# Kernel tuning notes

Measured on AMD Instinct MI355X. Metric: run time of the kernel, lower is better.

The kernel has to match this reference:

```python
import jax, jax.numpy as jnp
import numpy as np

N = 100000
E = 1600000
F_IN = 128
HID = 64
HEADS = 2
OUT_HEADS = 1
NUM_CLASS = 18
NEG_SLOPE = 0.2


def setup_inputs() -> dict:
    key = jax.random.key(0)
    ks = jax.random.split(key, 12)
    x = jax.random.normal(ks[0], (N, F_IN), dtype=jnp.float32)
    edge_index = jax.random.randint(ks[1], (2, E), 0, N, dtype=jnp.int64)
    s = lambda k, shp, fan: jax.random.normal(k, shp, dtype=jnp.float32) * (1.0 / np.sqrt(fan))
    W0 = s(ks[2], (F_IN, HID), F_IN)
    b0 = jnp.zeros((HID,), dtype=jnp.float32)
    W1 = s(ks[3], (HID, HEADS * HID), HID)
    att_src1 = s(ks[4], (HEADS, HID), HID)
    att_dst1 = s(ks[5], (HEADS, HID), HID)
    b1 = jnp.zeros((HEADS * HID,), dtype=jnp.float32)
    W2 = s(ks[6], (HEADS * HID, OUT_HEADS * NUM_CLASS), HEADS * HID)
    att_src2 = s(ks[7], (OUT_HEADS, NUM_CLASS), NUM_CLASS)
    att_dst2 = s(ks[8], (OUT_HEADS, NUM_CLASS), NUM_CLASS)
    b2 = jnp.zeros((OUT_HEADS * NUM_CLASS,), dtype=jnp.float32)
    return {"x": x, "edge_index": edge_index, "W0": W0, "b0": b0,
            "W1": W1, "att_src1": att_src1, "att_dst1": att_dst1, "b1": b1,
            "W2": W2, "att_src2": att_src2, "att_dst2": att_dst2, "b2": b2}


def gat_conv(x, src, dst, W, att_s, att_d, bias, heads, out_ch):
    n = x.shape[0]
    h = (x @ W).reshape(n, heads, out_ch)              # [N,H,C]
    a_s = jnp.sum(h * att_s, axis=-1)                   # [N,H]
    a_d = jnp.sum(h * att_d, axis=-1)                   # [N,H]
    e = jax.nn.leaky_relu(a_s[src] + a_d[dst], NEG_SLOPE)  # [E,H]
    m = jax.ops.segment_max(e, dst, num_segments=n)
    ex = jnp.exp(e - m[dst])
    denom = jax.ops.segment_sum(ex, dst, num_segments=n)
    alpha = ex / denom[dst]                              # [E,H]
    msg = h[src] * alpha[:, :, None]                     # [E,H,C]
    out = jax.ops.segment_sum(msg, dst, num_segments=n)  # [N,H,C]
    return out.reshape(n, heads * out_ch) + bias


def reference(x, edge_index, W0, b0, W1, att_src1, att_dst1, b1, W2, att_src2, att_dst2, b2):
    n = x.shape[0]
    # PyG GATConv adds self-loops by default
    loops = jnp.arange(n, dtype=edge_index.dtype)
    src = jnp.concatenate([edge_index[0], loops])
    dst = jnp.concatenate([edge_index[1], loops])
    # eval mode: dropout is identity
    h = jax.nn.relu(x @ W0 + b0)
    h = jax.nn.elu(gat_conv(h, src, dst, W1, att_src1, att_dst1, b1, HEADS, HID))
    out = gat_conv(h, src, dst, W2, att_src2, att_dst2, b2, OUT_HEADS, NUM_CLASS)
    return jax.nn.log_softmax(out, axis=-1)
```

## Files before the change

kernel.cpp:

```cpp
#include <hip/hip_runtime.h>
#include <math.h>


#define NEG_SLOPE 0.2f
#define STASH_CAP 128

typedef unsigned short ushort_t;

__device__ __forceinline__ float wmax(float v) {
    for (int o = 32; o; o >>= 1) v = fmaxf(v, __shfl_xor(v, o));
    return v;
}
__device__ __forceinline__ float wsum(float v) {
    for (int o = 32; o; o >>= 1) v += __shfl_xor(v, o);
    return v;
}

__device__ __forceinline__ unsigned bfpack(float a, float b) {
    unsigned ua = __float_as_uint(a);
    unsigned ub = __float_as_uint(b);
    ua = (ua + 0x7fffu + ((ua >> 16) & 1u)) >> 16;
    ub = (ub + 0x7fffu + ((ub >> 16) & 1u)) & 0xffff0000u;
    return ua | ub;
}
__device__ __forceinline__ ushort_t bf16of(float a) {
    unsigned ua = __float_as_uint(a);
    return (ushort_t)((ua + 0x7fffu + ((ua >> 16) & 1u)) >> 16);
}
__device__ __forceinline__ float bflo(unsigned u) { return __uint_as_float(u << 16); }
__device__ __forceinline__ float bfhi(unsigned u) { return __uint_as_float(u & 0xffff0000u); }
__device__ __forceinline__ float bfval(ushort_t u) { return __uint_as_float(((unsigned)u) << 16); }

__global__ void k_deg_init(int* __restrict__ deg, int N) {
    int i = blockIdx.x * blockDim.x + threadIdx.x;
    if (i < N) deg[i] = 1;
}
__global__ void k_deg_edges(const int* __restrict__ ei, int* __restrict__ deg,
                            int* __restrict__ eofs, int E) {
    int e = blockIdx.x * blockDim.x + threadIdx.x;
    if (e < E) eofs[e] = atomicAdd(&deg[ei[E + e]], 1);
}

__global__ __launch_bounds__(256) void k_scan1(const int* __restrict__ deg, int* __restrict__ rs,
                                               int* __restrict__ bsum, int N) {
    __shared__ int s[256];
    int t = threadIdx.x;
    int base = blockIdx.x * 1024;
    int i0 = base + t * 4;
    int d0 = (i0 + 0 < N) ? deg[i0 + 0] : 0;
    int d1 = (i0 + 1 < N) ? deg[i0 + 1] : 0;
    int d2 = (i0 + 2 < N) ? deg[i0 + 2] : 0;
    int d3 = (i0 + 3 < N) ? deg[i0 + 3] : 0;
    int s0 = d0, s1 = s0 + d1, s2 = s1 + d2, s3 = s2 + d3;
    int tsum = s3;
    s[t] = tsum;
    __syncthreads();
    for (int off = 1; off < 256; off <<= 1) {
        int v = (t >= off) ? s[t - off] : 0;
        __syncthreads();
        s[t] += v;
        __syncthreads();
    }
    int excl = s[t] - tsum;
    if (i0 + 0 < N) rs[1 + i0 + 0] = excl + s0;
    if (i0 + 1 < N) rs[1 + i0 + 1] = excl + s1;
    if (i0 + 2 < N) rs[1 + i0 + 2] = excl + s2;
    if (i0 + 3 < N) rs[1 + i0 + 3] = excl + s3;
    if (t == 0) bsum[blockIdx.x] = s[255];
}

__global__ __launch_bounds__(256) void k_scan2(const int* __restrict__ bsum,
                                               int* __restrict__ boff, int NB) {
    __shared__ int s[256];
    int t = threadIdx.x;
    int orig = (t < NB) ? bsum[t] : 0;
    s[t] = orig;
    __syncthreads();
    for (int off = 1; off < 256; off <<= 1) {
        int v = (t >= off) ? s[t - off] : 0;
        __syncthreads();
        s[t] += v;
        __syncthreads();
    }
    if (t < NB) boff[t] = s[t] - orig;
}

__global__ void k_scan3(int* __restrict__ rs, const int* __restrict__ boff, int N) {
    int i = blockIdx.x * blockDim.x + threadIdx.x;
    if (i == 0) rs[0] = 0;
    if (i < N) rs[1 + i] += boff[i >> 10];
}

__global__ __launch_bounds__(256) void k_scatter(const int* __restrict__ ei,
                                                 const int* __restrict__ eofs,
                                                 const int* __restrict__ rs,
                                                 int* __restrict__ csr,
                                                 int E, int Etot, int cohortBlocks) {
    int c = blockIdx.x & 7;
    int pb = blockIdx.x >> 3;
    int tid = pb * 256 + threadIdx.x;
    int stride = cohortBlocks * 256;
    for (int e = tid; e < Etot; e += stride) {
        int dst = (e < E) ? ei[E + e] : (e - E);
        if (((dst >> 13) & 7) != c) continue;
        int src, ofs;
        if (e < E) { src = ei[e]; ofs = eofs[e]; } else { src = dst; ofs = 0; }
        csr[rs[dst] + ofs] = src;
    }
}


__global__ __launch_bounds__(256) void k_gemm1(const float* __restrict__ x,
                                               const float* __restrict__ W0,
                                               const float* __restrict__ b0,
                                               unsigned* __restrict__ h0b, int N) {
    __shared__ float wl[128 * 64];
    __shared__ float al[64 * 132];
    int t = threadIdx.x;
    int n0 = blockIdx.x * 64;
    const float4* wg = (const float4*)W0;
    float4* wl4 = (float4*)wl;
#pragma unroll
    for (int i = 0; i < 8; ++i) wl4[t + i * 256] = wg[t + i * 256];
#pragma unroll
    for (int i = 0; i < 8; ++i) {
        int f = t + i * 256;
        int node = f >> 5, q = f & 31;
        int ng = n0 + node; if (ng > N - 1) ng = N - 1;
        float4 v = ((const float4*)x)[(size_t)ng * 32 + q];
        *(float4*)&al[node * 132 + q * 4] = v;
    }
    __syncthreads();
    int colg = t & 15;
    int rowg = t >> 4;
    float4 acc[4];
#pragma unroll
    for (int j = 0; j < 4; ++j) acc[j] = make_float4(0.f, 0.f, 0.f, 0.f);
    for (int k4 = 0; k4 < 128; k4 += 4) {
        float4 w0 = *(float4*)&wl[(k4 + 0) * 64 + colg * 4];
        float4 w1 = *(float4*)&wl[(k4 + 1) * 64 + colg * 4];
        float4 w2 = *(float4*)&wl[(k4 + 2) * 64 + colg * 4];
        float4 w3 = *(float4*)&wl[(k4 + 3) * 64 + colg * 4];
#pragma unroll
        for (int j = 0; j < 4; ++j) {
            float4 a = *(float4*)&al[(rowg * 4 + j) * 132 + k4];
            acc[j].x += a.x * w0.x + a.y * w1.x + a.z * w2.x + a.w * w3.x;
            acc[j].y += a.x * w0.y + a.y * w1.y + a.z * w2.y + a.w * w3.y;
            acc[j].z += a.x * w0.z + a.y * w1.z + a.z * w2.z + a.w * w3.z;
            acc[j].w += a.x * w0.w + a.y * w1.w + a.z * w2.w + a.w * w3.w;
        }
    }
    float4 bb = ((const float4*)b0)[colg];
#pragma unroll
    for (int j = 0; j < 4; ++j) {
        int n = n0 + rowg * 4 + j;
        if (n < N) {
            float rx = fmaxf(acc[j].x + bb.x, 0.f);
            float ry = fmaxf(acc[j].y + bb.y, 0.f);
            float rz = fmaxf(acc[j].z + bb.z, 0.f);
            float rw = fmaxf(acc[j].w + bb.w, 0.f);
            uint2 pr; pr.x = bfpack(rx, ry); pr.y = bfpack(rz, rw);
            ((uint2*)h0b)[(size_t)n * 16 + colg] = pr;
        }
    }
}

__global__ __launch_bounds__(256) void k_gemm2(const unsigned* __restrict__ h0b,
                                               const float* __restrict__ W1,
                                               const float* __restrict__ as_g,
                                               const float* __restrict__ ad_g,
                                               ushort_t* __restrict__ h1b,
                                               float* __restrict__ as1,
                                               float* __restrict__ ad1, int N) {
    __shared__ float wl[64 * 128];
    __shared__ float al[64 * 68];
    int t = threadIdx.x;
    int n0 = blockIdx.x * 64;
    const float4* wg = (const float4*)W1;
    float4* wl4 = (float4*)wl;
#pragma unroll
    for (int i = 0; i < 8; ++i) wl4[t + i * 256] = wg[t + i * 256];
#pragma unroll
    for (int i = 0; i < 2; ++i) {
        int f = t + i * 256;
        int node = f >> 3, q = f & 7;
        int ng = n0 + node; if (ng > N - 1) ng = N - 1;
        uint4 u = ((const uint4*)h0b)[(size_t)ng * 8 + q];
        float* dst = &al[node * 68 + q * 8];
        dst[0] = bflo(u.x); dst[1] = bfhi(u.x);
        dst[2] = bflo(u.y); dst[3] = bfhi(u.y);
        dst[4] = bflo(u.z); dst[5] = bfhi(u.z);
        dst[6] = bflo(u.w); dst[7] = bfhi(u.w);
    }
    __syncthreads();
    int colg = t & 31;
    int rowg = t >> 5;
    float4 acc[8];
#pragma unroll
    for (int j = 0; j < 8; ++j) acc[j] = make_float4(0.f, 0.f, 0.f, 0.f);
    for (int k4 = 0; k4 < 64; k4 += 4) {
        float4 w0 = *(float4*)&wl[(k4 + 0) * 128 + colg * 4];
        float4 w1 = *(float4*)&wl[(k4 + 1) * 128 + colg * 4];
        float4 w2 = *(float4*)&wl[(k4 + 2) * 128 + colg * 4];
        float4 w3 = *(float4*)&wl[(k4 + 3) * 128 + colg * 4];
#pragma unroll
        for (int j = 0; j < 8; ++j) {
            float4 a = *(float4*)&al[(rowg * 8 + j) * 68 + k4];
            acc[j].x += a.x * w0.x + a.y * w1.x + a.z * w2.x + a.w * w3.x;
            acc[j].y += a.x * w0.y + a.y * w1.y + a.z * w2.y + a.w * w3.y;
            acc[j].z += a.x * w0.z + a.y * w1.z + a.z * w2.z + a.w * w3.z;
            acc[j].w += a.x * w0.w + a.y * w1.w + a.z * w2.w + a.w * w3.w;
        }
    }
    float4 asv = ((const float4*)as_g)[colg];
    float4 adv = ((const float4*)ad_g)[colg];
    float ps[8], pd[8];
#pragma unroll
    for (int j = 0; j < 8; ++j) {
        ps[j] = acc[j].x * asv.x + acc[j].y * asv.y + acc[j].z * asv.z + acc[j].w * asv.w;
        pd[j] = acc[j].x * adv.x + acc[j].y * adv.y + acc[j].z * adv.z + acc[j].w * adv.w;
    }
    for (int o = 1; o < 16; o <<= 1) {
#pragma unroll
        for (int j = 0; j < 8; ++j) {
            ps[j] += __shfl_xor(ps[j], o);
            pd[j] += __shfl_xor(pd[j], o);
        }
    }
#pragma unroll
    for (int j = 0; j < 8; ++j) {
        int n = n0 + rowg * 8 + j;
        if (n < N) {
            uint2 pr;
            pr.x = bfpack(acc[j].x, acc[j].y);
            pr.y = bfpack(acc[j].z, acc[j].w);
            ((uint2*)h1b)[(size_t)n * 32 + colg] = pr;
        }
    }
    int lane = t & 63;
    if ((lane & 15) == 0) {
        int head = (lane >> 4) & 1;
#pragma unroll
        for (int j = 0; j < 8; ++j) {
            int n = n0 + rowg * 8 + j;
            if (n < N) {
                as1[n * 2 + head] = ps[j];
                ad1[n * 2 + head] = pd[j];
            }
        }
    }
}

__global__ __launch_bounds__(256) void k_node_l1(const int* __restrict__ rs,
                                                 const int* __restrict__ csr,
                                                 const ushort_t* __restrict__ h1b,
                                                 const float* __restrict__ as1,
                                                 const float* __restrict__ ad1,
                                                 const float* __restrict__ b1,
                                                 unsigned* __restrict__ aggb, int N) {
    __shared__ float2 stashA[4][128];
    __shared__ float4 stashE[4][STASH_CAP];
    int wid = threadIdx.x >> 6;
    int lane = threadIdx.x & 63;
    int n = (blockIdx.x * 256 + threadIdx.x) >> 6;
    if (n >= N) return;
    int row = rs[n], end = rs[n + 1];
    int deg = end - row;
    float2 adv = ((const float2*)ad1)[n];
    const float2* asp = (const float2*)as1;
    const char* h1base = (const char*)h1b;
    int eg = lane >> 4;
    int fl = lane & 15;
    int head_off = (fl >= 8) ? 64 : 0;
    int flbase = fl * 16;
    float acc[8] = {0.f, 0.f, 0.f, 0.f, 0.f, 0.f, 0.f, 0.f};
    float inv0, inv1;
    if (deg <= 64) {
        bool act = lane < deg;
        int src = act ? csr[row + lane] : 0;
        float2 av = asp[src];
        float e0 = av.x + adv.x, e1 = av.y + adv.y;
        e0 = e0 > 0.f ? e0 : NEG_SLOPE * e0;
        e1 = e1 > 0.f ? e1 : NEG_SLOPE * e1;
        if (!act) { e0 = -INFINITY; e1 = -INFINITY; }
        float m0 = wmax(e0), m1 = wmax(e1);
        float p0 = act ? __expf(e0 - m0) : 0.f;
        float p1 = act ? __expf(e1 - m1) : 0.f;
        inv0 = __builtin_amdgcn_rcpf(wsum(p0));
        inv1 = __builtin_amdgcn_rcpf(wsum(p1));
        stashA[wid][lane] = make_float2(__int_as_float(src), p0);
        stashA[wid][64 + lane] = make_float2(__int_as_float(src), p1);
        int deg8 = (deg + 7) & ~7;
        int b0i = head_off + eg;
        float2 sa0 = stashA[wid][b0i];
        float2 sa1 = stashA[wid][b0i + 4];
        uint4 u0 = *(const uint4*)(h1base + (((unsigned)__float_as_int(sa0.x)) << 8) + flbase);
        uint4 u1 = *(const uint4*)(h1base + (((unsigned)__float_as_int(sa1.x)) << 8) + flbase);
        for (int j = 0; j < deg8; j += 8) {
            int jn = (j + 8 < deg8) ? j + 8 : 0;
            float2 sb0 = stashA[wid][b0i + jn];
            float2 sb1 = stashA[wid][b0i + jn + 4];
            uint4 v0 = *(const uint4*)(h1base + (((unsigned)__float_as_int(sb0.x)) << 8) + flbase);
            uint4 v1 = *(const uint4*)(h1base + (((unsigned)__float_as_int(sb1.x)) << 8) + flbase);
            float a0 = sa0.y, a1 = sa1.y;
            acc[0] += bflo(u0.x) * a0; acc[1] += bfhi(u0.x) * a0;
            acc[2] += bflo(u0.y) * a0; acc[3] += bfhi(u0.y) * a0;
            acc[4] += bflo(u0.z) * a0; acc[5] += bfhi(u0.z) * a0;
            acc[6] += bflo(u0.w) * a0; acc[7] += bfhi(u0.w) * a0;
            acc[0] += bflo(u1.x) * a1; acc[1] += bfhi(u1.x) * a1;
            acc[2] += bflo(u1.y) * a1; acc[3] += bfhi(u1.y) * a1;
            acc[4] += bflo(u1.z) * a1; acc[5] += bfhi(u1.z) * a1;
            acc[6] += bflo(u1.w) * a1; acc[7] += bfhi(u1.w) * a1;
            sa0 = sb0; sa1 = sb1; u0 = v0; u1 = v1;
        }
    } else {
        inv0 = 1.f; inv1 = 1.f;
        float m0 = -INFINITY, m1 = -INFINITY, l0 = 0.f, l1 = 0.f;
        for (int base = row; base < end; base += 64) {
            int idx = base + lane;
            bool act = idx < end;
            int src = act ? csr[idx] : 0;
            float2 av = asp[src];
            float e0 = av.x + adv.x, e1 = av.y + adv.y;
            e0 = e0 > 0.f ? e0 : NEG_SLOPE * e0;
            e1 = e1 > 0.f ? e1 : NEG_SLOPE * e1;
            int sidx = idx - row;
            if (act && sidx < STASH_CAP)
                stashE[wid][sidx] = make_float4(__int_as_float(src), e0, e1, 0.f);
            if (!act) { e0 = -INFINITY; e1 = -INFINITY; }
            float m0n = fmaxf(m0, wmax(e0));
            float m1n = fmaxf(m1, wmax(e1));
            float p0 = act ? __expf(e0 - m0n) : 0.f;
            float p1 = act ? __expf(e1 - m1n) : 0.f;
            l0 = l0 * __expf(m0 - m0n) + wsum(p0);
            l1 = l1 * __expf(m1 - m1n) + wsum(p1);
            m0 = m0n; m1 = m1n;
        }
        float r0 = __builtin_amdgcn_rcpf(l0);
        float r1 = __builtin_amdgcn_rcpf(l1);
        for (int base = row; base < end; base += 64) {
            int idx = base + lane;
            bool act = idx < end;
            int sidx = idx - row;
            int src; float e0, e1;
            if (sidx < STASH_CAP) {
                float4 se = stashE[wid][sidx];
                src = __float_as_int(se.x);
                e0 = se.y; e1 = se.z;
            } else {
                src = act ? csr[idx] : 0;
                float2 av = asp[src];
                e0 = av.x + adv.x; e1 = av.y + adv.y;
                e0 = e0 > 0.f ? e0 : NEG_SLOPE * e0;
                e1 = e1 > 0.f ? e1 : NEG_SLOPE * e1;
            }
            if (!act) src = 0;
            float a0 = act ? __expf(e0 - m0) * r0 : 0.f;
            float a1 = act ? __expf(e1 - m1) * r1 : 0.f;
            stashA[wid][lane] = make_float2(__int_as_float(src), a0);
            stashA[wid][64 + lane] = make_float2(__int_as_float(src), a1);
            int cnt = min(64, end - base);
            for (int j = 0; j < cnt; j += 4) {
                float2 sa = stashA[wid][head_off + j + eg];
                int sj = __float_as_int(sa.x);
                float aj = sa.y;
                uint4 u = *(const uint4*)(h1base + (((unsigned)sj) << 8) + flbase);
                acc[0] += bflo(u.x) * aj; acc[1] += bfhi(u.x) * aj;
                acc[2] += bflo(u.y) * aj; acc[3] += bfhi(u.y) * aj;
                acc[4] += bflo(u.z) * aj; acc[5] += bfhi(u.z) * aj;
                acc[6] += bflo(u.w) * aj; acc[7] += bfhi(u.w) * aj;
            }
        }
    }
#pragma unroll
    for (int i = 0; i < 8; ++i) {
        acc[i] += __shfl_xor(acc[i], 16);
        acc[i] += __shfl_xor(acc[i], 32);
    }
    if (lane < 16) {
        float inv = (lane >= 8) ? inv1 : inv0;
        float4 ba = ((const float4*)b1)[lane * 2];
        float4 bb4 = ((const float4*)b1)[lane * 2 + 1];
        float v[8];
        v[0] = acc[0] * inv + ba.x;  v[1] = acc[1] * inv + ba.y;
        v[2] = acc[2] * inv + ba.z;  v[3] = acc[3] * inv + ba.w;
        v[4] = acc[4] * inv + bb4.x; v[5] = acc[5] * inv + bb4.y;
        v[6] = acc[6] * inv + bb4.z; v[7] = acc[7] * inv + bb4.w;
#pragma unroll
        for (int i = 0; i < 8; ++i) v[i] = v[i] > 0.f ? v[i] : __expf(v[i]) - 1.f;
        uint4 pk;
        pk.x = bfpack(v[0], v[1]); pk.y = bfpack(v[2], v[3]);
        pk.z = bfpack(v[4], v[5]); pk.w = bfpack(v[6], v[7]);
        ((uint4*)aggb)[(size_t)n * 16 + lane] = pk;
    }
}

__global__ __launch_bounds__(256, 4) void k_node2(const unsigned* __restrict__ aggb,
                                                  const float* __restrict__ W2,
                                                  const float* __restrict__ as_g,
                                                  const float* __restrict__ ad_g,
                                                  ushort_t* __restrict__ h2b,
                                                  float* __restrict__ a_s,
                                                  float* __restrict__ a_d, int N) {
    __shared__ float al[64 * 132];
    __shared__ float w2t[20 * 132];
    int t = threadIdx.x;
    int n0 = blockIdx.x * 64;
#pragma unroll
    for (int i = 0; i < 4; ++i) {
        int f = t + i * 256;
        int node = f >> 4, q = f & 15;
        int ng = n0 + node; if (ng > N - 1) ng = N - 1;
        uint4 u = ((const uint4*)aggb)[(size_t)ng * 16 + q];
        float* dst = &al[node * 132 + q * 8];
        dst[0] = bflo(u.x); dst[1] = bfhi(u.x);
        dst[2] = bflo(u.y); dst[3] = bfhi(u.y);
        dst[4] = bflo(u.z); dst[5] = bfhi(u.z);
        dst[6] = bflo(u.w); dst[7] = bfhi(u.w);
    }
    for (int i = t; i < 2560; i += 256) {
        int c = i >> 7, k = i & 127;
        w2t[c * 132 + k] = (c < 18) ? W2[k * 18 + c] : 0.f;
    }
    __syncthreads();
    int node = t >> 2;
    int cq = t & 3;
    int c0 = cq * 5;
    int n = n0 + node;
    float acc[5] = {0.f, 0.f, 0.f, 0.f, 0.f};
#pragma unroll 2
    for (int k4 = 0; k4 < 128; k4 += 4) {
        float4 a = *(float4*)&al[node * 132 + k4];
#pragma unroll
        for (int i = 0; i < 5; ++i) {
            float4 w = *(float4*)&w2t[(c0 + i) * 132 + k4];
            acc[i] += a.x * w.x + a.y * w.y + a.z * w.z + a.w * w.w;
        }
    }
    float ps = 0.f, pd = 0.f;
#pragma unroll
    for (int i = 0; i < 5; ++i) {
        int c = c0 + i;
        float asv = (c < 18) ? as_g[c] : 0.f;
        float adv = (c < 18) ? ad_g[c] : 0.f;
        ps += acc[i] * asv;
        pd += acc[i] * adv;
    }
    ps += __shfl_xor(ps, 1); ps += __shfl_xor(ps, 2);
    pd += __shfl_xor(pd, 1); pd += __shfl_xor(pd, 2);
    if (n < N) {
#pragma unroll
        for (int i = 0; i < 5; ++i) {
            int c = c0 + i;
            if (c < 18) h2b[(size_t)n * 32 + c] = bf16of(acc[i]);
        }
        if (cq == 0) { a_s[n] = ps; a_d[n] = pd; }
    }
}

__global__ __launch_bounds__(256) void k_node_l2(const int* __restrict__ rs,
                                                 const int* __restrict__ csr,
                                                 const ushort_t* __restrict__ h2b,
                                                 const float* __restrict__ as2,
                                                 const float* __restrict__ ad2,
                                                 const float* __restrict__ b2,
                                                 float* __restrict__ out, int N) {
    __shared__ float2 stash[4][STASH_CAP];
    int wid = threadIdx.x >> 6;
    int lane = threadIdx.x & 63;
    int n = (blockIdx.x * 256 + threadIdx.x) >> 6;
    if (n >= N) return;
    int row = rs[n], end = rs[n + 1];
    int deg = end - row;
    float adn = ad2[n];
    int g = lane / 21;
    int c = lane - g * 21;
    int cc = c < 18 ? c : 17;
    float acc = 0.f;
    float post;
    if (deg <= 64) {
        bool act = lane < deg;
        int src = act ? csr[row + lane] : 0;
        float e = as2[src] + adn;
        e = e > 0.f ? e : NEG_SLOPE * e;
        if (!act) e = -INFINITY;
        float m = wmax(e);
        float p = act ? __expf(e - m) : 0.f;
        post = __builtin_amdgcn_rcpf(wsum(p));
        stash[wid][lane] = make_float2(__int_as_float(src), p);
        int o = g;
        for (; o + 3 < deg; o += 6) {
            float2 s0 = stash[wid][o];
            float2 s1 = stash[wid][o + 3];
            int q0 = __float_as_int(s0.x);
            int q1 = __float_as_int(s1.x);
            float v0 = bfval(h2b[(size_t)q0 * 32 + cc]);
            float v1 = bfval(h2b[(size_t)q1 * 32 + cc]);
            acc += s0.y * v0 + s1.y * v1;
        }
        if (o < deg) {
            float2 s0 = stash[wid][o];
            int q0 = __float_as_int(s0.x);
            acc += s0.y * bfval(h2b[(size_t)q0 * 32 + cc]);
        }
    } else {
        post = 1.f;
        float m = -INFINITY, l = 0.f;
        for (int base = row; base < end; base += 64) {
            int idx = base + lane;
            bool act = idx < end;
            int src = act ? csr[idx] : 0;
            float e = as2[src] + adn;
            e = e > 0.f ? e : NEG_SLOPE * e;
            int sidx = idx - row;
            if (act && sidx < STASH_CAP)
                stash[wid][sidx] = make_float2(__int_as_float(src), e);
            if (!act) e = -INFINITY;
            float mn = fmaxf(m, wmax(e));
            float p = act ? __expf(e - mn) : 0.f;
            l = l * __expf(m - mn) + wsum(p);
            m = mn;
        }
        float invl = __builtin_amdgcn_rcpf(l);
        int lim = deg < STASH_CAP ? deg : STASH_CAP;
        for (int o = g; o < lim; o += 3) {
            float2 se = stash[wid][o];
            int src = __float_as_int(se.x);
            float alpha = __expf(se.y - m) * invl;
            acc += alpha * bfval(h2b[(size_t)src * 32 + cc]);
        }
        for (int pos = row + STASH_CAP + g; pos < end; pos += 3) {
            int src = csr[pos];
            float e = as2[src] + adn;
            e = e > 0.f ? e : NEG_SLOPE * e;
            float alpha = __expf(e - m) * invl;
            acc += alpha * bfval(h2b[(size_t)src * 32 + cc]);
        }
    }
    float t1 = __shfl(acc, (lane + 21) & 63);
    float t2 = __shfl(acc, (lane + 42) & 63);
    acc += t1 + t2;
    float bb = (lane < 18) ? b2[lane] : 0.f;
    float v = acc * post + bb;
    float tmx = (lane < 18) ? v : -INFINITY;
    for (int o = 16; o; o >>= 1) tmx = fmaxf(tmx, __shfl_xor(tmx, o));
    float s = (lane < 18) ? __expf(v - tmx) : 0.f;
    for (int o = 16; o; o >>= 1) s += __shfl_xor(s, o);
    float lse = tmx + __logf(s);
    if (lane < 18) out[(size_t)n * 18 + lane] = v - lse;
}

extern "C" void kernel_launch(void* const* d_in, const int* in_sizes, int n_in,
                              void* d_out, int out_size, void* d_ws, size_t ws_size,
                              hipStream_t stream) {
    const float* x      = (const float*)d_in[0];
    const int*   ei     = (const int*)d_in[1];
    const float* W0     = (const float*)d_in[2];
    const float* b0     = (const float*)d_in[3];
    const float* W1     = (const float*)d_in[4];
    const float* att_s1 = (const float*)d_in[5];
    const float* att_d1 = (const float*)d_in[6];
    const float* b1     = (const float*)d_in[7];
    const float* W2     = (const float*)d_in[8];
    const float* att_s2 = (const float*)d_in[9];
    const float* att_d2 = (const float*)d_in[10];
    const float* b2     = (const float*)d_in[11];

    const int N = in_sizes[0] / 128;
    const int E = in_sizes[1] / 2;
    const int Etot = E + N;
    const int NB = (N + 1023) / 1024;
    const int NBLK = (N + 63) / 64;

    char* w = (char*)d_ws;
    unsigned* h0b  = (unsigned*)w; w += (size_t)N * 64 * 2;
    ushort_t* h1b  = (ushort_t*)w; w += (size_t)N * 128 * 2;
    unsigned* aggb = (unsigned*)w; w += (size_t)N * 128 * 2;
    float* as1     = (float*)w;    w += (size_t)N * 2 * 4;
    float* ad1     = (float*)w;    w += (size_t)N * 2 * 4;
    ushort_t* h2b  = (ushort_t*)w; w += (size_t)N * 32 * 2;
    float* as2     = (float*)w;    w += (size_t)N * 4;
    float* ad2     = (float*)w;    w += (size_t)N * 4;
    int* deg       = (int*)w;      w += (size_t)N * 4;
    int* rs        = (int*)w;      w += (size_t)(N + 1) * 4;
    int* bsum      = (int*)w;      w += (size_t)256 * 4;
    int* boff      = (int*)w;      w += (size_t)256 * 4;
    int* eofs      = (int*)w;      w += (size_t)E * 4;
    int* csr       = (int*)w;      w += (size_t)Etot * 4;

    float* out = (float*)d_out;

    k_deg_init<<<(N + 255) / 256, 256, 0, stream>>>(deg, N);
    k_deg_edges<<<(E + 255) / 256, 256, 0, stream>>>(ei, deg, eofs, E);
    k_scan1<<<NB, 256, 0, stream>>>(deg, rs, bsum, N);
    k_scan2<<<1, 256, 0, stream>>>(bsum, boff, NB);
    k_scan3<<<(N + 255) / 256, 256, 0, stream>>>(rs, boff, N);
    const int cohortBlocks = 128;
    k_scatter<<<8 * cohortBlocks, 256, 0, stream>>>(ei, eofs, rs, csr, E, Etot, cohortBlocks);

    k_gemm1<<<NBLK, 256, 0, stream>>>(x, W0, b0, h0b, N);
    k_gemm2<<<NBLK, 256, 0, stream>>>(h0b, W1, att_s1, att_d1, h1b, as1, ad1, N);

    k_node_l1<<<(N * 64 + 255) / 256, 256, 0, stream>>>(rs, csr, h1b, as1, ad1, b1, aggb, N);

    k_node2<<<NBLK, 256, 0, stream>>>(aggb, W2, att_s2, att_d2, h2b, as2, ad2, N);
    k_node_l2<<<(N * 64 + 255) / 256, 256, 0, stream>>>(rs, csr, h2b, as2, ad2, b2, out, N);
}
```

Measured before the change: 433.9 us.

## Fuse two input GEMMs and replace per-edge offsets with cursor-based CSR scatter

The first two dense layers now run in one kernel. The ReLU output of the first GEMM stays in shared memory in fp32 instead of round-tripping through a bf16 global buffer. The CSR build drops the per-edge offset array: degree counting uses dst-cohort blocks, and the scatter claims slots by atomically incrementing a per-node cursor. This removes global traffic and a launch, at the cost of more atomics in the scatter and a nondeterministic neighbor order within each row. It also changes numerics slightly, since the hidden layer is no longer rounded to bf16.

```diff
diff --git a/kernel.cpp b/kernel.cpp
--- a/kernel.cpp
+++ b/kernel.cpp
@@ -35,10 +35,19 @@
     int i = blockIdx.x * blockDim.x + threadIdx.x;
     if (i < N) deg[i] = 1;
 }
-__global__ void k_deg_edges(const int* __restrict__ ei, int* __restrict__ deg,
-                            int* __restrict__ eofs, int E) {
-    int e = blockIdx.x * blockDim.x + threadIdx.x;
-    if (e < E) eofs[e] = atomicAdd(&deg[ei[E + e]], 1);
+
+__global__ __launch_bounds__(256) void k_deg_edges(const int* __restrict__ ei,
+                                                   int* __restrict__ deg,
+                                                   int E, int cohortBlocks) {
+    int c = blockIdx.x & 7;
+    int pb = blockIdx.x >> 3;
+    int tid = pb * 256 + threadIdx.x;
+    int stride = cohortBlocks * 256;
+    for (int e = tid; e < E; e += stride) {
+        int dst = ei[E + e];
+        if (((dst >> 13) & 7) != c) continue;
+        atomicAdd(&deg[dst], 1);
+    }
 }
 
 __global__ __launch_bounds__(256) void k_scan1(const int* __restrict__ deg, int* __restrict__ rs,
@@ -85,14 +94,19 @@
     if (t < NB) boff[t] = s[t] - orig;
 }
 
-__global__ void k_scan3(int* __restrict__ rs, const int* __restrict__ boff, int N) {
+__global__ void k_scan3(int* __restrict__ rs, const int* __restrict__ boff,
+                        const int* __restrict__ deg, int* __restrict__ cursor, int N) {
     int i = blockIdx.x * blockDim.x + threadIdx.x;
     if (i == 0) rs[0] = 0;
-    if (i < N) rs[1 + i] += boff[i >> 10];
+    if (i < N) {
+        int v = rs[1 + i] + boff[i >> 10];
+        rs[1 + i] = v;
+        cursor[i] = v - deg[i] + 1;
+    }
 }
 
 __global__ __launch_bounds__(256) void k_scatter(const int* __restrict__ ei,
-                                                 const int* __restrict__ eofs,
+                                                 int* __restrict__ cursor,
                                                  const int* __restrict__ rs,
                                                  int* __restrict__ csr,
                                                  int E, int Etot, int cohortBlocks) {
@@ -103,32 +117,43 @@
     for (int e = tid; e < Etot; e += stride) {
         int dst = (e < E) ? ei[E + e] : (e - E);
         if (((dst >> 13) & 7) != c) continue;
-        int src, ofs;
-        if (e < E) { src = ei[e]; ofs = eofs[e]; } else { src = dst; ofs = 0; }
-        csr[rs[dst] + ofs] = src;
-    }
-}
-
-
-__global__ __launch_bounds__(256) void k_gemm1(const float* __restrict__ x,
-                                               const float* __restrict__ W0,
-                                               const float* __restrict__ b0,
-                                               unsigned* __restrict__ h0b, int N) {
-    __shared__ float wl[128 * 64];
-    __shared__ float al[64 * 132];
+        if (e < E) {
+            int pos = atomicAdd(&cursor[dst], 1);
+            csr[pos] = ei[e];
+        } else {
+            csr[rs[dst]] = dst;
+        }
+    }
+}
+
+__global__ __launch_bounds__(256) void k_gemm12(const float* __restrict__ x,
+                                                const float* __restrict__ W0,
+                                                const float* __restrict__ b0,
+                                                const float* __restrict__ W1,
+                                                const float* __restrict__ as_g,
+                                                const float* __restrict__ ad_g,
+                                                ushort_t* __restrict__ h1b,
+                                                float* __restrict__ as1,
+                                                float* __restrict__ ad1, int N) {
+    __shared__ float smem[16640];
+    float* al  = smem;
+    float* wl  = smem + 8448;
+    float* al2 = smem;
     int t = threadIdx.x;
     int n0 = blockIdx.x * 64;
-    const float4* wg = (const float4*)W0;
-    float4* wl4 = (float4*)wl;
-#pragma unroll
-    for (int i = 0; i < 8; ++i) wl4[t + i * 256] = wg[t + i * 256];
-#pragma unroll
-    for (int i = 0; i < 8; ++i) {
-        int f = t + i * 256;
-        int node = f >> 5, q = f & 31;
-        int ng = n0 + node; if (ng > N - 1) ng = N - 1;
-        float4 v = ((const float4*)x)[(size_t)ng * 32 + q];
-        *(float4*)&al[node * 132 + q * 4] = v;
+    {
+        const float4* wg = (const float4*)W0;
+        float4* wl4 = (float4*)wl;
+#pragma unroll
+        for (int i = 0; i < 8; ++i) wl4[t + i * 256] = wg[t + i * 256];
+#pragma unroll
+        for (int i = 0; i < 8; ++i) {
+            int f = t + i * 256;
+            int node = f >> 5, q = f & 31;
+            int ng = n0 + node; if (ng > N - 1) ng = N - 1;
+            float4 v = ((const float4*)x)[(size_t)ng * 32 + q];
+            *(float4*)&al[node * 132 + q * 4] = v;
+        }
     }
     __syncthreads();
     int colg = t & 15;
@@ -151,74 +176,51 @@
         }
     }
     float4 bb = ((const float4*)b0)[colg];
+    float4 h0v[4];
 #pragma unroll
     for (int j = 0; j < 4; ++j) {
-        int n = n0 + rowg * 4 + j;
-        if (n < N) {
-            float rx = fmaxf(acc[j].x + bb.x, 0.f);
-            float ry = fmaxf(acc[j].y + bb.y, 0.f);
-            float rz = fmaxf(acc[j].z + bb.z, 0.f);
-            float rw = fmaxf(acc[j].w + bb.w, 0.f);
-            uint2 pr; pr.x = bfpack(rx, ry); pr.y = bfpack(rz, rw);
-            ((uint2*)h0b)[(size_t)n * 16 + colg] = pr;
-        }
-    }
-}
-
-__global__ __launch_bounds__(256) void k_gemm2(const unsigned* __restrict__ h0b,
-                                               const float* __restrict__ W1,
-                                               const float* __restrict__ as_g,
-                                               const float* __restrict__ ad_g,
-                                               ushort_t* __restrict__ h1b,
-                                               float* __restrict__ as1,
-                                               float* __restrict__ ad1, int N) {
-    __shared__ float wl[64 * 128];
-    __shared__ float al[64 * 68];
-    int t = threadIdx.x;
-    int n0 = blockIdx.x * 64;
-    const float4* wg = (const float4*)W1;
-    float4* wl4 = (float4*)wl;
-#pragma unroll
-    for (int i = 0; i < 8; ++i) wl4[t + i * 256] = wg[t + i * 256];
-#pragma unroll
-    for (int i = 0; i < 2; ++i) {
-        int f = t + i * 256;
-        int node = f >> 3, q = f & 7;
-        int ng = n0 + node; if (ng > N - 1) ng = N - 1;
-        uint4 u = ((const uint4*)h0b)[(size_t)ng * 8 + q];
-        float* dst = &al[node * 68 + q * 8];
-        dst[0] = bflo(u.x); dst[1] = bfhi(u.x);
-        dst[2] = bflo(u.y); dst[3] = bfhi(u.y);
-        dst[4] = bflo(u.z); dst[5] = bfhi(u.z);
-        dst[6] = bflo(u.w); dst[7] = bfhi(u.w);
+        h0v[j].x = fmaxf(acc[j].x + bb.x, 0.f);
+        h0v[j].y = fmaxf(acc[j].y + bb.y, 0.f);
+        h0v[j].z = fmaxf(acc[j].z + bb.z, 0.f);
+        h0v[j].w = fmaxf(acc[j].w + bb.w, 0.f);
     }
     __syncthreads();
-    int colg = t & 31;
-    int rowg = t >> 5;
-    float4 acc[8];
-#pragma unroll
-    for (int j = 0; j < 8; ++j) acc[j] = make_float4(0.f, 0.f, 0.f, 0.f);
+#pragma unroll
+    for (int j = 0; j < 4; ++j)
+        *(float4*)&al2[(rowg * 4 + j) * 68 + colg * 4] = h0v[j];
+    {
+        const float4* wg1 = (const float4*)W1;
+        float4* wl4 = (float4*)wl;
+#pragma unroll
+        for (int i = 0; i < 8; ++i) wl4[t + i * 256] = wg1[t + i * 256];
+    }
+    __syncthreads();
+    int colg2 = t & 31;
+    int rowg2 = t >> 5;
+    float4 acc2[8];
+#pragma unroll
+    for (int j = 0; j < 8; ++j) acc2[j] = make_float4(0.f, 0.f, 0.f, 0.f);
     for (int k4 = 0; k4 < 64; k4 += 4) {
-        float4 w0 = *(float4*)&wl[(k4 + 0) * 128 + colg * 4];
-        float4 w1 = *(float4*)&wl[(k4 + 1) * 128 + colg * 4];
-        float4 w2 = *(float4*)&wl[(k4 + 2) * 128 + colg * 4];
-        float4 w3 = *(float4*)&wl[(k4 + 3) * 128 + colg * 4];
+        float4 w0 = *(float4*)&wl[(k4 + 0) * 128 + colg2 * 4];
+        float4 w1 = *(float4*)&wl[(k4 + 1) * 128 + colg2 * 4];
+        float4 w2 = *(float4*)&wl[(k4 + 2) * 128 + colg2 * 4];
+        float4 w3 = *(float4*)&wl[(k4 + 3) * 128 + colg2 * 4];
 #pragma unroll
         for (int j = 0; j < 8; ++j) {
-            float4 a = *(float4*)&al[(rowg * 8 + j) * 68 + k4];
-            acc[j].x += a.x * w0.x + a.y * w1.x + a.z * w2.x + a.w * w3.x;
-            acc[j].y += a.x * w0.y + a.y * w1.y + a.z * w2.y + a.w * w3.y;
-            acc[j].z += a.x * w0.z + a.y * w1.z + a.z * w2.z + a.w * w3.z;
-            acc[j].w += a.x * w0.w + a.y * w1.w + a.z * w2.w + a.w * w3.w;
-        }
-    }
-    float4 asv = ((const float4*)as_g)[colg];
-    float4 adv = ((const float4*)ad_g)[colg];
+            float4 a = *(float4*)&al2[(rowg2 * 8 + j) * 68 + k4];
+            acc2[j].x += a.x * w0.x + a.y * w1.x + a.z * w2.x + a.w * w3.x;
+            acc2[j].y += a.x * w0.y + a.y * w1.y + a.z * w2.y + a.w * w3.y;
+            acc2[j].z += a.x * w0.z + a.y * w1.z + a.z * w2.z + a.w * w3.z;
+            acc2[j].w += a.x * w0.w + a.y * w1.w + a.z * w2.w + a.w * w3.w;
+        }
+    }
+    float4 asv = ((const float4*)as_g)[colg2];
+    float4 adv = ((const float4*)ad_g)[colg2];
     float ps[8], pd[8];
 #pragma unroll
     for (int j = 0; j < 8; ++j) {
-        ps[j] = acc[j].x * asv.x + acc[j].y * asv.y + acc[j].z * asv.z + acc[j].w * asv.w;
-        pd[j] = acc[j].x * adv.x + acc[j].y * adv.y + acc[j].z * adv.z + acc[j].w * adv.w;
+        ps[j] = acc2[j].x * asv.x + acc2[j].y * asv.y + acc2[j].z * asv.z + acc2[j].w * asv.w;
+        pd[j] = acc2[j].x * adv.x + acc2[j].y * adv.y + acc2[j].z * adv.z + acc2[j].w * adv.w;
     }
     for (int o = 1; o < 16; o <<= 1) {
 #pragma unroll
@@ -229,12 +231,12 @@
     }
 #pragma unroll
     for (int j = 0; j < 8; ++j) {
-        int n = n0 + rowg * 8 + j;
+        int n = n0 + rowg2 * 8 + j;
         if (n < N) {
             uint2 pr;
-            pr.x = bfpack(acc[j].x, acc[j].y);
-            pr.y = bfpack(acc[j].z, acc[j].w);
-            ((uint2*)h1b)[(size_t)n * 32 + colg] = pr;
+            pr.x = bfpack(acc2[j].x, acc2[j].y);
+            pr.y = bfpack(acc2[j].z, acc2[j].w);
+            ((uint2*)h1b)[(size_t)n * 32 + colg2] = pr;
         }
     }
     int lane = t & 63;
@@ -242,7 +244,7 @@
         int head = (lane >> 4) & 1;
 #pragma unroll
         for (int j = 0; j < 8; ++j) {
-            int n = n0 + rowg * 8 + j;
+            int n = n0 + rowg2 * 8 + j;
             if (n < N) {
                 as1[n * 2 + head] = ps[j];
                 ad1[n * 2 + head] = pd[j];
@@ -573,7 +575,6 @@
     const int NBLK = (N + 63) / 64;
 
     char* w = (char*)d_ws;
-    unsigned* h0b  = (unsigned*)w; w += (size_t)N * 64 * 2;
     ushort_t* h1b  = (ushort_t*)w; w += (size_t)N * 128 * 2;
     unsigned* aggb = (unsigned*)w; w += (size_t)N * 128 * 2;
     float* as1     = (float*)w;    w += (size_t)N * 2 * 4;
@@ -583,23 +584,23 @@
     float* ad2     = (float*)w;    w += (size_t)N * 4;
     int* deg       = (int*)w;      w += (size_t)N * 4;
     int* rs        = (int*)w;      w += (size_t)(N + 1) * 4;
+    int* cursor    = (int*)w;      w += (size_t)N * 4;
     int* bsum      = (int*)w;      w += (size_t)256 * 4;
     int* boff      = (int*)w;      w += (size_t)256 * 4;
-    int* eofs      = (int*)w;      w += (size_t)E * 4;
     int* csr       = (int*)w;      w += (size_t)Etot * 4;
 
     float* out = (float*)d_out;
 
+    const int cohortBlocks = 128;
+
     k_deg_init<<<(N + 255) / 256, 256, 0, stream>>>(deg, N);
-    k_deg_edges<<<(E + 255) / 256, 256, 0, stream>>>(ei, deg, eofs, E);
+    k_deg_edges<<<8 * cohortBlocks, 256, 0, stream>>>(ei, deg, E, cohortBlocks);
     k_scan1<<<NB, 256, 0, stream>>>(deg, rs, bsum, N);
     k_scan2<<<1, 256, 0, stream>>>(bsum, boff, NB);
-    k_scan3<<<(N + 255) / 256, 256, 0, stream>>>(rs, boff, N);
-    const int cohortBlocks = 128;
-    k_scatter<<<8 * cohortBlocks, 256, 0, stream>>>(ei, eofs, rs, csr, E, Etot, cohortBlocks);
-
-    k_gemm1<<<NBLK, 256, 0, stream>>>(x, W0, b0, h0b, N);
-    k_gemm2<<<NBLK, 256, 0, stream>>>(h0b, W1, att_s1, att_d1, h1b, as1, ad1, N);
+    k_scan3<<<(N + 255) / 256, 256, 0, stream>>>(rs, boff, deg, cursor, N);
+    k_scatter<<<8 * cohortBlocks, 256, 0, stream>>>(ei, cursor, rs, csr, E, Etot, cohortBlocks);
+
+    k_gemm12<<<NBLK, 256, 0, stream>>>(x, W0, b0, W1, att_s1, att_d1, h1b, as1, ad1, N);
 
     k_node_l1<<<(N * 64 + 255) / 256, 256, 0, stream>>>(rs, csr, h1b, as1, ad1, b1, aggb, N);
 
```

After: 462.8 us. 1.07x slower.
